# Optimization experiments

Hardware: AMD Instinct MI355X
Metric: run time of the kernel (lower is better)

## Reference

```python
import jax, jax.numpy as jnp
import numpy as np

NEG_SLOPE = 0.2
MASK_FILL = -9e10


def setup_inputs() -> dict:
    key = jax.random.key(0)
    ks = jax.random.split(key, 9)
    B, n_ope, n_mac = 32, 2048, 1024
    total = 64
    ope_dim, mac_dim, out_dim = 64, 64, 128
    ope_ma_adj = jax.random.randint(ks[0], (total, n_ope, n_mac), 0, 2, dtype=jnp.int32)
    batch_idxes = jax.random.randint(ks[1], (B,), 0, total, dtype=jnp.int64)
    feat_ope = jax.random.normal(ks[2], (B, n_ope, ope_dim), dtype=jnp.float32)
    feat_mac = jax.random.normal(ks[3], (B, n_mac, mac_dim), dtype=jnp.float32)
    # parameters (xavier-normal-like scaling)
    def xavier(k, shape):
        fan_in, fan_out = shape[1], shape[0]
        std = jnp.sqrt(2.0 / (fan_in + fan_out))
        return std * jax.random.normal(k, shape, dtype=jnp.float32)
    ope_w = xavier(ks[4], (out_dim, ope_dim))   # Linear weight [out, in]
    mac_w = xavier(ks[5], (out_dim, mac_dim))
    ope_alpha = xavier(ks[6], (out_dim, 1))
    mac_alpha = xavier(ks[7], (out_dim, 1))
    res_w = xavier(ks[8], (out_dim, mac_dim))
    return {
        "ope_ma_adj": ope_ma_adj, "batch_idxes": batch_idxes,
        "feat_ope": feat_ope, "feat_mac": feat_mac,
        "ope_w": ope_w, "mac_w": mac_w,
        "ope_alpha": ope_alpha, "mac_alpha": mac_alpha, "res_w": res_w,
    }


def reference(ope_ma_adj, batch_idxes, feat_ope, feat_mac,
              ope_w, mac_w, ope_alpha, mac_alpha, res_w):
    # dropout p=0 -> identity
    h_ope = jnp.einsum('bod,kd->bok', feat_ope, ope_w)   # [B, n_ope, out]
    h_mac = jnp.einsum('bmd,kd->bmk', feat_mac, mac_w)   # [B, n_mac, out]
    attn_ope = jnp.einsum('bok,k->bo', h_ope, ope_alpha[:, 0])  # [B, n_ope]
    attn_mac = jnp.einsum('bmk,k->bm', h_mac, mac_alpha[:, 0])  # [B, n_mac]
    e = attn_ope[:, :, None] + attn_mac[:, None, :]             # [B, n_ope, n_mac]
    e = jnp.where(e >= 0, e, NEG_SLOPE * e)                      # leaky relu
    mask = ope_ma_adj[batch_idxes] == 1                          # [B, n_ope, n_mac]
    e = jnp.where(mask, e, MASK_FILL)
    alpha = jax.nn.softmax(e, axis=-2)                           # over operations
    out = jnp.einsum('bom,bok->bmk', alpha, h_ope)               # [B, n_mac, out]
    h_res = jnp.einsum('bmd,kd->bmk', feat_mac, res_w)
    return out + h_res
```

## Files before the change

kernel.cpp:

```cpp
#include <hip/hip_runtime.h>

#define N_OPE 2048
#define N_MAC 1024
#define DIM   64
#define KOUT  128
#define NB    32

typedef __attribute__((ext_vector_type(8))) short short8;
typedef __attribute__((ext_vector_type(4))) float floatx4;

static __device__ __forceinline__ unsigned short f2bf(float f) {
    unsigned int u = __builtin_bit_cast(unsigned int, f);
    u += 0x7fffu + ((u >> 16) & 1u);
    return (unsigned short)(u >> 16);
}
static __device__ __forceinline__ float bf2f(unsigned short h) {
    unsigned int u = ((unsigned int)h) << 16;
    return __builtin_bit_cast(float, u);
}

__global__ __launch_bounds__(256, 2) void k_ope(const float* __restrict__ feat,
        const float* __restrict__ w, const float* __restrict__ alpha,
        unsigned short* __restrict__ h_t, float2* __restrict__ pq)
{
    int wid = threadIdx.x >> 6, lane = threadIdx.x & 63;
    int L = lane & 15, q = lane >> 4;
    int base = blockIdx.x * 128 + wid * 32;
    int b = base >> 11;
    int o0w = base & (N_OPE - 1);

    float fA[2][2][8];
    #pragma unroll
    for (int mf = 0; mf < 2; ++mf) {
        const float* fr = feat + (size_t)(base + mf * 16 + L) * DIM + q * 8;
        #pragma unroll
        for (int ks = 0; ks < 2; ++ks) {
            float4 v0 = *(const float4*)(fr + ks * 32);
            float4 v1 = *(const float4*)(fr + ks * 32 + 4);
            fA[mf][ks][0] = v0.x; fA[mf][ks][1] = v0.y; fA[mf][ks][2] = v0.z; fA[mf][ks][3] = v0.w;
            fA[mf][ks][4] = v1.x; fA[mf][ks][5] = v1.y; fA[mf][ks][6] = v1.z; fA[mf][ks][7] = v1.w;
        }
    }

    short8 Ah[2][2], Al[2][2];
    #pragma unroll
    for (int mf = 0; mf < 2; ++mf)
        #pragma unroll
        for (int ks = 0; ks < 2; ++ks)
            #pragma unroll
            for (int j = 0; j < 8; ++j) {
                float x = fA[mf][ks][j];
                unsigned short h = f2bf(x);
                Ah[mf][ks][j] = (short)h;
                Al[mf][ks][j] = (short)f2bf(x - bf2f(h));
            }

    floatx4 C[2][8];
    #pragma unroll
    for (int mf = 0; mf < 2; ++mf)
        #pragma unroll
        for (int nf = 0; nf < 8; ++nf) C[mf][nf] = (floatx4)0.f;

    #pragma unroll
    for (int ks = 0; ks < 2; ++ks) {
        #pragma unroll
        for (int nf = 0; nf < 8; ++nf) {
            const float* wp = w + (size_t)(nf * 16 + L) * DIM + ks * 32 + q * 8;
            float4 u0 = *(const float4*)(wp);
            float4 u1 = *(const float4*)(wp + 4);
            float bw[8] = {u0.x, u0.y, u0.z, u0.w, u1.x, u1.y, u1.z, u1.w};
            short8 Bh, Bl;
            #pragma unroll
            for (int j = 0; j < 8; ++j) {
                unsigned short h = f2bf(bw[j]);
                Bh[j] = (short)h;
                Bl[j] = (short)f2bf(bw[j] - bf2f(h));
            }
            #pragma unroll
            for (int mf = 0; mf < 2; ++mf) {
                C[mf][nf] = __builtin_amdgcn_mfma_f32_16x16x32_bf16(Ah[mf][ks], Bh, C[mf][nf], 0, 0, 0);
                C[mf][nf] = __builtin_amdgcn_mfma_f32_16x16x32_bf16(Al[mf][ks], Bh, C[mf][nf], 0, 0, 0);
                C[mf][nf] = __builtin_amdgcn_mfma_f32_16x16x32_bf16(Ah[mf][ks], Bl, C[mf][nf], 0, 0, 0);
            }
        }
    }

    float alf[8];
    #pragma unroll
    for (int nf = 0; nf < 8; ++nf) alf[nf] = alpha[nf * 16 + L];
    #pragma unroll
    for (int mf = 0; mf < 2; ++mf) {
        #pragma unroll
        for (int r = 0; r < 4; ++r) {
            float s = 0.f;
            #pragma unroll
            for (int nf = 0; nf < 8; ++nf) s = fmaf(C[mf][nf][r], alf[nf], s);
            s += __shfl_xor(s, 1); s += __shfl_xor(s, 2);
            s += __shfl_xor(s, 4); s += __shfl_xor(s, 8);
            if (L == 0)
                pq[base + mf * 16 + q * 4 + r] = make_float2(__expf(s), __expf(0.2f * s));
        }
    }

    __shared__ unsigned short T[4][128 * 34];
    #pragma unroll
    for (int mf = 0; mf < 2; ++mf)
        #pragma unroll
        for (int nf = 0; nf < 8; ++nf)
            #pragma unroll
            for (int r = 0; r < 4; ++r)
                T[wid][(nf * 16 + L) * 34 + mf * 16 + q * 4 + r] = f2bf(C[mf][nf][r]);
    __syncthreads();
    unsigned short* htb = h_t + (size_t)b * KOUT * N_OPE;
    #pragma unroll 4
    for (int t = 0; t < 32; ++t) {
        int n = t * 4 + q;
        ushort2 v = *(const ushort2*)&T[wid][n * 34 + 2 * L];
        *(ushort2*)(htb + (size_t)n * N_OPE + o0w + 2 * L) = v;
    }
}

__global__ __launch_bounds__(256, 3) void k_attn(const int* __restrict__ adj,
        const int* __restrict__ bidx,
        const unsigned short* __restrict__ h_t,
        const float2* __restrict__ pq,
        const float* __restrict__ feat_mac,
        const float* __restrict__ mac_w, const float* __restrict__ mac_alpha,
        const float* __restrict__ res_w,
        float* __restrict__ out)
{
    int b  = blockIdx.y;
    int m0 = blockIdx.x * 32;
    int t  = threadIdx.x;
    int wv = t >> 6;
    int lane = t & 63;
    int L = lane & 15, q = lane >> 4;

    __shared__ float buf0[32 * 132];
    __shared__ float buf1[32 * 132];
    __shared__ float waS[64];
    __shared__ float amS[32];
    __shared__ float DS[4][32];

    {
        int d = t & 63, seg = t >> 6;
        float p = 0.f;
        #pragma unroll 8
        for (int n = seg * 32; n < seg * 32 + 32; ++n)
            p = fmaf(mac_w[n * DIM + d], mac_alpha[n], p);
        buf0[seg * 64 + d] = p;
    }
    __syncthreads();
    if (t < 64) waS[t] = buf0[t] + buf0[64 + t] + buf0[128 + t] + buf0[192 + t];
    __syncthreads();
    {
        int row = t & 31, seg = t >> 5;
        const float* fr = feat_mac + ((size_t)b * N_MAC + m0 + row) * DIM + seg * 8;
        float p = 0.f;
        #pragma unroll
        for (int k = 0; k < 8; ++k) p = fmaf(fr[k], waS[seg * 8 + k], p);
        buf1[seg * 32 + row] = p;
    }
    __syncthreads();
    if (t < 32) {
        float s = 0.f;
        #pragma unroll
        for (int sg = 0; sg < 8; ++sg) s += buf1[sg * 32 + t];
        amS[t] = s;
    }
    __syncthreads();

    float am0 = amS[L], am1 = amS[16 + L];
    float pM0 = __expf(am0), qM0 = __expf(0.2f * am0);
    float pM1 = __expf(am1), qM1 = __expf(0.2f * am1);

    const int* adjt = adj + (size_t)bidx[b] * N_OPE * N_MAC;
    const unsigned short* htb = h_t + (size_t)b * KOUT * N_OPE;
    const float2* pqb = pq + (size_t)b * N_OPE;

    floatx4 C0[8], C1[8];
    #pragma unroll
    for (int i = 0; i < 8; ++i) { C0[i] = (floatx4)0.f; C1[i] = (floatx4)0.f; }
    float den0 = 0.f, den1 = 0.f;

    int oBeg = wv * (N_OPE / 4);
    for (int o0 = oBeg; o0 < oBeg + N_OPE / 4; o0 += 32) {
        int ob = o0 + q * 8;
        float4 pv0 = *(const float4*)(pqb + ob);
        float4 pv1 = *(const float4*)(pqb + ob + 2);
        float4 pv2 = *(const float4*)(pqb + ob + 4);
        float4 pv3 = *(const float4*)(pqb + ob + 6);
        float pA[8] = {pv0.x, pv0.z, pv1.x, pv1.z, pv2.x, pv2.z, pv3.x, pv3.z};
        float qA[8] = {pv0.y, pv0.w, pv1.y, pv1.w, pv2.y, pv2.w, pv3.y, pv3.w};

        short8 Bf[8];
        #pragma unroll
        for (int nf = 0; nf < 8; ++nf)
            Bf[nf] = *(const short8*)(htb + (size_t)(nf * 16 + L) * N_OPE + ob);

        int mk0[8], mk1[8];
        #pragma unroll
        for (int j = 0; j < 8; ++j) {
            mk0[j] = adjt[(size_t)(ob + j) * N_MAC + m0 + L];
            mk1[j] = adjt[(size_t)(ob + j) * N_MAC + m0 + 16 + L];
        }

        float w0v[8], w1v[8];
        #pragma unroll
        for (int j = 0; j < 8; ++j) {
            float tp0 = pA[j] * pM0;
            float w0 = (tp0 >= 1.0f) ? tp0 : qA[j] * qM0;
            w0 = (mk0[j] == 1) ? w0 : 0.f;
            den0 += w0; w0v[j] = w0;
            float tp1 = pA[j] * pM1;
            float w1 = (tp1 >= 1.0f) ? tp1 : qA[j] * qM1;
            w1 = (mk1[j] == 1) ? w1 : 0.f;
            den1 += w1; w1v[j] = w1;
        }
        int4 A0i, A1i;
        #pragma unroll
        for (int j2 = 0; j2 < 4; ++j2) {
            unsigned lo0 = __builtin_bit_cast(unsigned, w0v[2 * j2])     + 0x8000u;
            unsigned hi0 = __builtin_bit_cast(unsigned, w0v[2 * j2 + 1]) + 0x8000u;
            ((unsigned*)&A0i)[j2] = __builtin_amdgcn_perm(hi0, lo0, 0x07060302u);
            unsigned lo1 = __builtin_bit_cast(unsigned, w1v[2 * j2])     + 0x8000u;
            unsigned hi1 = __builtin_bit_cast(unsigned, w1v[2 * j2 + 1]) + 0x8000u;
            ((unsigned*)&A1i)[j2] = __builtin_amdgcn_perm(hi1, lo1, 0x07060302u);
        }
        short8 A0 = __builtin_bit_cast(short8, A0i);
        short8 A1 = __builtin_bit_cast(short8, A1i);

        #pragma unroll
        for (int nf = 0; nf < 8; ++nf) {
            C0[nf] = __builtin_amdgcn_mfma_f32_16x16x32_bf16(A0, Bf[nf], C0[nf], 0, 0, 0);
            C1[nf] = __builtin_amdgcn_mfma_f32_16x16x32_bf16(A1, Bf[nf], C1[nf], 0, 0, 0);
        }
    }

    den0 += __shfl_xor(den0, 16); den0 += __shfl_xor(den0, 32);
    den1 += __shfl_xor(den1, 16); den1 += __shfl_xor(den1, 32);
    if (q == 0) { DS[wv][L] = den0; DS[wv][16 + L] = den1; }

    if (wv == 0 || wv == 2) {
        float* bp = (wv == 0) ? buf0 : buf1;
        #pragma unroll
        for (int mf = 0; mf < 2; ++mf) {
            const floatx4* Cf = mf ? C1 : C0;
            #pragma unroll
            for (int nf = 0; nf < 8; ++nf)
                #pragma unroll
                for (int r = 0; r < 4; ++r)
                    bp[(mf * 16 + q * 4 + r) * 132 + nf * 16 + L] = Cf[nf][r];
        }
    }
    __syncthreads();
    if (wv == 1 || wv == 3) {
        float* bp = (wv == 1) ? buf0 : buf1;
        #pragma unroll
        for (int mf = 0; mf < 2; ++mf) {
            const floatx4* Cf = mf ? C1 : C0;
            #pragma unroll
            for (int nf = 0; nf < 8; ++nf)
                #pragma unroll
                for (int r = 0; r < 4; ++r)
                    bp[(mf * 16 + q * 4 + r) * 132 + nf * 16 + L] += Cf[nf][r];
        }
    }
    __syncthreads();

    float fA[2][2][8];
    #pragma unroll
    for (int mf = 0; mf < 2; ++mf) {
        const float* fr = feat_mac + ((size_t)b * N_MAC + m0 + mf * 16 + L) * DIM + q * 8;
        #pragma unroll
        for (int ks = 0; ks < 2; ++ks) {
            float4 v0 = *(const float4*)(fr + ks * 32);
            float4 v1 = *(const float4*)(fr + ks * 32 + 4);
            fA[mf][ks][0] = v0.x; fA[mf][ks][1] = v0.y; fA[mf][ks][2] = v0.z; fA[mf][ks][3] = v0.w;
            fA[mf][ks][4] = v1.x; fA[mf][ks][5] = v1.y; fA[mf][ks][6] = v1.z; fA[mf][ks][7] = v1.w;
        }
    }
    short8 Ah[2][2], Al[2][2];
    #pragma unroll
    for (int mf = 0; mf < 2; ++mf)
        #pragma unroll
        for (int ks = 0; ks < 2; ++ks)
            #pragma unroll
            for (int j = 0; j < 8; ++j) {
                float x = fA[mf][ks][j];
                unsigned short h = f2bf(x);
                Ah[mf][ks][j] = (short)h;
                Al[mf][ks][j] = (short)f2bf(x - bf2f(h));
            }
    floatx4 R[2][2];
    R[0][0] = (floatx4)0.f; R[0][1] = (floatx4)0.f;
    R[1][0] = (floatx4)0.f; R[1][1] = (floatx4)0.f;
    #pragma unroll
    for (int ks = 0; ks < 2; ++ks) {
        #pragma unroll
        for (int nfl = 0; nfl < 2; ++nfl) {
            const float* wp = res_w + (size_t)((wv * 2 + nfl) * 16 + L) * DIM + ks * 32 + q * 8;
            float4 u0 = *(const float4*)(wp);
            float4 u1 = *(const float4*)(wp + 4);
            float bw[8] = {u0.x, u0.y, u0.z, u0.w, u1.x, u1.y, u1.z, u1.w};
            short8 Bh, Bl;
            #pragma unroll
            for (int j = 0; j < 8; ++j) {
                unsigned short h = f2bf(bw[j]);
                Bh[j] = (short)h;
                Bl[j] = (short)f2bf(bw[j] - bf2f(h));
            }
            #pragma unroll
            for (int mf = 0; mf < 2; ++mf) {
                R[mf][nfl] = __builtin_amdgcn_mfma_f32_16x16x32_bf16(Ah[mf][ks], Bh, R[mf][nfl], 0, 0, 0);
                R[mf][nfl] = __builtin_amdgcn_mfma_f32_16x16x32_bf16(Al[mf][ks], Bh, R[mf][nfl], 0, 0, 0);
                R[mf][nfl] = __builtin_amdgcn_mfma_f32_16x16x32_bf16(Ah[mf][ks], Bl, R[mf][nfl], 0, 0, 0);
            }
        }
    }

    #pragma unroll
    for (int mf = 0; mf < 2; ++mf) {
        #pragma unroll
        for (int r = 0; r < 4; ++r) {
            int row = mf * 16 + q * 4 + r;
            float inv = 1.0f / (DS[0][row] + DS[1][row] + DS[2][row] + DS[3][row]);
            size_t obase = ((size_t)b * N_MAC + m0 + row) * KOUT;
            #pragma unroll
            for (int nfl = 0; nfl < 2; ++nfl) {
                int col = (wv * 2 + nfl) * 16 + L;
                out[obase + col] = (buf0[row * 132 + col] + buf1[row * 132 + col]) * inv
                                   + R[mf][nfl][r];
            }
        }
    }
}

extern "C" void kernel_launch(void* const* d_in, const int* in_sizes, int n_in,
                              void* d_out, int out_size, void* d_ws, size_t ws_size,
                              hipStream_t stream) {
    const int*   adj       = (const int*)d_in[0];
    const int*   bidx      = (const int*)d_in[1];
    const float* feat_ope  = (const float*)d_in[2];
    const float* feat_mac  = (const float*)d_in[3];
    const float* ope_w     = (const float*)d_in[4];
    const float* mac_w     = (const float*)d_in[5];
    const float* ope_alpha = (const float*)d_in[6];
    const float* mac_alpha = (const float*)d_in[7];
    const float* res_w     = (const float*)d_in[8];
    float* out = (float*)d_out;

    char* ws = (char*)d_ws;
    unsigned short* h_t = (unsigned short*)ws;
    float2* pq          = (float2*)(ws + (size_t)(16 << 20));

    k_ope<<<512, 256, 0, stream>>>(feat_ope, ope_w, ope_alpha, h_t, pq);
    k_attn<<<dim3(N_MAC / 32, NB), 256, 0, stream>>>(adj, bidx, h_t, pq, feat_mac,
                                                     mac_w, mac_alpha, res_w, out);
}
```

Baseline: 718.5 us.

## Split mac projection and residual into separate kernels, vectorize adjacency loads

The per-machine attention scalar and the residual projection move out of the attention kernel. A tiny kernel precomputes mac_w^T·mac_alpha, and a new k_mac kernel writes attn_mac plus the residual directly into out. The attention kernel drops its shared-memory prologue and residual MFMA tail; it now adds into out and loads adjacency as int2, with each lane owning two adjacent machine columns. The grid becomes a 1D launch with a remapped batch order and relaxed launch bounds. The cost is two extra launches and an extra read-modify-write of out.

```diff
diff --git a/kernel.cpp b/kernel.cpp
--- a/kernel.cpp
+++ b/kernel.cpp
@@ -17,6 +17,16 @@
 static __device__ __forceinline__ float bf2f(unsigned short h) {
     unsigned int u = ((unsigned int)h) << 16;
     return __builtin_bit_cast(float, u);
+}
+
+__global__ void k_wa(const float* __restrict__ mw, const float* __restrict__ ma,
+                     float* __restrict__ wa)
+{
+    int d = threadIdx.x;
+    float s = 0.f;
+    #pragma unroll 8
+    for (int n = 0; n < KOUT; ++n) s = fmaf(mw[n * DIM + d], ma[n], s);
+    wa[d] = s;
 }
 
 __global__ __launch_bounds__(256, 2) void k_ope(const float* __restrict__ feat,
@@ -120,63 +130,122 @@
     }
 }
 
-__global__ __launch_bounds__(256, 3) void k_attn(const int* __restrict__ adj,
+__global__ __launch_bounds__(256, 2) void k_mac(const float* __restrict__ feat,
+        const float* __restrict__ w, const float* __restrict__ wa,
+        float* __restrict__ out, float* __restrict__ attn)
+{
+    int wid = threadIdx.x >> 6, lane = threadIdx.x & 63;
+    int L = lane & 15, q = lane >> 4;
+    int base = blockIdx.x * 128 + wid * 32;
+
+    float fA[2][2][8];
+    #pragma unroll
+    for (int mf = 0; mf < 2; ++mf) {
+        const float* fr = feat + (size_t)(base + mf * 16 + L) * DIM + q * 8;
+        #pragma unroll
+        for (int ks = 0; ks < 2; ++ks) {
+            float4 v0 = *(const float4*)(fr + ks * 32);
+            float4 v1 = *(const float4*)(fr + ks * 32 + 4);
+            fA[mf][ks][0] = v0.x; fA[mf][ks][1] = v0.y; fA[mf][ks][2] = v0.z; fA[mf][ks][3] = v0.w;
+            fA[mf][ks][4] = v1.x; fA[mf][ks][5] = v1.y; fA[mf][ks][6] = v1.z; fA[mf][ks][7] = v1.w;
+        }
+    }
+
+    float wav[2][8];
+    #pragma unroll
+    for (int ks = 0; ks < 2; ++ks) {
+        float4 w0 = *(const float4*)(wa + ks * 32 + q * 8);
+        float4 w1 = *(const float4*)(wa + ks * 32 + q * 8 + 4);
+        wav[ks][0] = w0.x; wav[ks][1] = w0.y; wav[ks][2] = w0.z; wav[ks][3] = w0.w;
+        wav[ks][4] = w1.x; wav[ks][5] = w1.y; wav[ks][6] = w1.z; wav[ks][7] = w1.w;
+    }
+    float part[2] = {0.f, 0.f};
+    #pragma unroll
+    for (int mf = 0; mf < 2; ++mf)
+        #pragma unroll
+        for (int ks = 0; ks < 2; ++ks)
+            #pragma unroll
+            for (int j = 0; j < 8; ++j)
+                part[mf] = fmaf(fA[mf][ks][j], wav[ks][j], part[mf]);
+    part[0] += __shfl_xor(part[0], 16); part[0] += __shfl_xor(part[0], 32);
+    part[1] += __shfl_xor(part[1], 16); part[1] += __shfl_xor(part[1], 32);
+    if (q == 0) {
+        attn[base + L]      = part[0];
+        attn[base + 16 + L] = part[1];
+    }
+
+    short8 Ah[2][2], Al[2][2];
+    #pragma unroll
+    for (int mf = 0; mf < 2; ++mf)
+        #pragma unroll
+        for (int ks = 0; ks < 2; ++ks)
+            #pragma unroll
+            for (int j = 0; j < 8; ++j) {
+                float x = fA[mf][ks][j];
+                unsigned short h = f2bf(x);
+                Ah[mf][ks][j] = (short)h;
+                Al[mf][ks][j] = (short)f2bf(x - bf2f(h));
+            }
+
+    floatx4 C[2][8];
+    #pragma unroll
+    for (int mf = 0; mf < 2; ++mf)
+        #pragma unroll
+        for (int nf = 0; nf < 8; ++nf) C[mf][nf] = (floatx4)0.f;
+
+    #pragma unroll
+    for (int ks = 0; ks < 2; ++ks) {
+        #pragma unroll
+        for (int nf = 0; nf < 8; ++nf) {
+            const float* wp = w + (size_t)(nf * 16 + L) * DIM + ks * 32 + q * 8;
+            float4 u0 = *(const float4*)(wp);
+            float4 u1 = *(const float4*)(wp + 4);
+            float bw[8] = {u0.x, u0.y, u0.z, u0.w, u1.x, u1.y, u1.z, u1.w};
+            short8 Bh, Bl;
+            #pragma unroll
+            for (int j = 0; j < 8; ++j) {
+                unsigned short h = f2bf(bw[j]);
+                Bh[j] = (short)h;
+                Bl[j] = (short)f2bf(bw[j] - bf2f(h));
+            }
+            #pragma unroll
+            for (int mf = 0; mf < 2; ++mf) {
+                C[mf][nf] = __builtin_amdgcn_mfma_f32_16x16x32_bf16(Ah[mf][ks], Bh, C[mf][nf], 0, 0, 0);
+                C[mf][nf] = __builtin_amdgcn_mfma_f32_16x16x32_bf16(Al[mf][ks], Bh, C[mf][nf], 0, 0, 0);
+                C[mf][nf] = __builtin_amdgcn_mfma_f32_16x16x32_bf16(Ah[mf][ks], Bl, C[mf][nf], 0, 0, 0);
+            }
+        }
+    }
+
+    #pragma unroll
+    for (int mf = 0; mf < 2; ++mf)
+        #pragma unroll
+        for (int nf = 0; nf < 8; ++nf)
+            #pragma unroll
+            for (int r = 0; r < 4; ++r)
+                out[(size_t)(base + mf * 16 + q * 4 + r) * KOUT + nf * 16 + L] = C[mf][nf][r];
+}
+
+__global__ __launch_bounds__(256) void k_attn(const int* __restrict__ adj,
         const int* __restrict__ bidx,
         const unsigned short* __restrict__ h_t,
         const float2* __restrict__ pq,
-        const float* __restrict__ feat_mac,
-        const float* __restrict__ mac_w, const float* __restrict__ mac_alpha,
-        const float* __restrict__ res_w,
+        const float* __restrict__ attn_mac,
         float* __restrict__ out)
 {
-    int b  = blockIdx.y;
-    int m0 = blockIdx.x * 32;
-    int t  = threadIdx.x;
-    int wv = t >> 6;
-    int lane = t & 63;
+    int lin = blockIdx.x;
+    int b   = 4 * (lin & 7) + ((lin >> 3) & 3);
+    int m0  = (lin >> 5) * 32;
+    int t = threadIdx.x, wv = t >> 6, lane = t & 63;
     int L = lane & 15, q = lane >> 4;
 
-    __shared__ float buf0[32 * 132];
-    __shared__ float buf1[32 * 132];
-    __shared__ float waS[64];
-    __shared__ float amS[32];
-    __shared__ float DS[4][32];
-
-    {
-        int d = t & 63, seg = t >> 6;
-        float p = 0.f;
-        #pragma unroll 8
-        for (int n = seg * 32; n < seg * 32 + 32; ++n)
-            p = fmaf(mac_w[n * DIM + d], mac_alpha[n], p);
-        buf0[seg * 64 + d] = p;
-    }
-    __syncthreads();
-    if (t < 64) waS[t] = buf0[t] + buf0[64 + t] + buf0[128 + t] + buf0[192 + t];
-    __syncthreads();
-    {
-        int row = t & 31, seg = t >> 5;
-        const float* fr = feat_mac + ((size_t)b * N_MAC + m0 + row) * DIM + seg * 8;
-        float p = 0.f;
-        #pragma unroll
-        for (int k = 0; k < 8; ++k) p = fmaf(fr[k], waS[seg * 8 + k], p);
-        buf1[seg * 32 + row] = p;
-    }
-    __syncthreads();
-    if (t < 32) {
-        float s = 0.f;
-        #pragma unroll
-        for (int sg = 0; sg < 8; ++sg) s += buf1[sg * 32 + t];
-        amS[t] = s;
-    }
-    __syncthreads();
-
-    float am0 = amS[L], am1 = amS[16 + L];
-    float pM0 = __expf(am0), qM0 = __expf(0.2f * am0);
-    float pM1 = __expf(am1), qM1 = __expf(0.2f * am1);
-
-    const int* adjt = adj + (size_t)bidx[b] * N_OPE * N_MAC;
+    const int* adjt = adj + (size_t)bidx[b] * (N_OPE * N_MAC);
     const unsigned short* htb = h_t + (size_t)b * KOUT * N_OPE;
     const float2* pqb = pq + (size_t)b * N_OPE;
+
+    float2 amv = *(const float2*)(attn_mac + (size_t)b * N_MAC + m0 + 2 * L);
+    float pM0 = __expf(amv.x), qM0 = __expf(0.2f * amv.x);
+    float pM1 = __expf(amv.y), qM1 = __expf(0.2f * amv.y);
 
     floatx4 C0[8], C1[8];
     #pragma unroll
@@ -193,28 +262,26 @@
         float pA[8] = {pv0.x, pv0.z, pv1.x, pv1.z, pv2.x, pv2.z, pv3.x, pv3.z};
         float qA[8] = {pv0.y, pv0.w, pv1.y, pv1.w, pv2.y, pv2.w, pv3.y, pv3.w};
 
+        int2 mk[8];
+        #pragma unroll
+        for (int j = 0; j < 8; ++j)
+            mk[j] = *(const int2*)(adjt + (size_t)(ob + j) * N_MAC + m0 + 2 * L);
+
         short8 Bf[8];
         #pragma unroll
         for (int nf = 0; nf < 8; ++nf)
             Bf[nf] = *(const short8*)(htb + (size_t)(nf * 16 + L) * N_OPE + ob);
-
-        int mk0[8], mk1[8];
-        #pragma unroll
-        for (int j = 0; j < 8; ++j) {
-            mk0[j] = adjt[(size_t)(ob + j) * N_MAC + m0 + L];
-            mk1[j] = adjt[(size_t)(ob + j) * N_MAC + m0 + 16 + L];
-        }
 
         float w0v[8], w1v[8];
         #pragma unroll
         for (int j = 0; j < 8; ++j) {
             float tp0 = pA[j] * pM0;
             float w0 = (tp0 >= 1.0f) ? tp0 : qA[j] * qM0;
-            w0 = (mk0[j] == 1) ? w0 : 0.f;
+            w0 = (mk[j].x == 1) ? w0 : 0.f;
             den0 += w0; w0v[j] = w0;
             float tp1 = pA[j] * pM1;
             float w1 = (tp1 >= 1.0f) ? tp1 : qA[j] * qM1;
-            w1 = (mk1[j] == 1) ? w1 : 0.f;
+            w1 = (mk[j].y == 1) ? w1 : 0.f;
             den1 += w1; w1v[j] = w1;
         }
         int4 A0i, A1i;
@@ -239,6 +306,10 @@
 
     den0 += __shfl_xor(den0, 16); den0 += __shfl_xor(den0, 32);
     den1 += __shfl_xor(den1, 16); den1 += __shfl_xor(den1, 32);
+
+    __shared__ float buf0[32 * 132];
+    __shared__ float buf1[32 * 132];
+    __shared__ float DS[4][32];
     if (q == 0) { DS[wv][L] = den0; DS[wv][16 + L] = den1; }
 
     if (wv == 0 || wv == 2) {
@@ -268,69 +339,21 @@
     }
     __syncthreads();
 
-    float fA[2][2][8];
     #pragma unroll
     for (int mf = 0; mf < 2; ++mf) {
-        const float* fr = feat_mac + ((size_t)b * N_MAC + m0 + mf * 16 + L) * DIM + q * 8;
-        #pragma unroll
-        for (int ks = 0; ks < 2; ++ks) {
-            float4 v0 = *(const float4*)(fr + ks * 32);
-            float4 v1 = *(const float4*)(fr + ks * 32 + 4);
-            fA[mf][ks][0] = v0.x; fA[mf][ks][1] = v0.y; fA[mf][ks][2] = v0.z; fA[mf][ks][3] = v0.w;
-            fA[mf][ks][4] = v1.x; fA[mf][ks][5] = v1.y; fA[mf][ks][6] = v1.z; fA[mf][ks][7] = v1.w;
-        }
-    }
-    short8 Ah[2][2], Al[2][2];
-    #pragma unroll
-    for (int mf = 0; mf < 2; ++mf)
-        #pragma unroll
-        for (int ks = 0; ks < 2; ++ks)
-            #pragma unroll
-            for (int j = 0; j < 8; ++j) {
-                float x = fA[mf][ks][j];
-                unsigned short h = f2bf(x);
-                Ah[mf][ks][j] = (short)h;
-                Al[mf][ks][j] = (short)f2bf(x - bf2f(h));
-            }
-    floatx4 R[2][2];
-    R[0][0] = (floatx4)0.f; R[0][1] = (floatx4)0.f;
-    R[1][0] = (floatx4)0.f; R[1][1] = (floatx4)0.f;
-    #pragma unroll
-    for (int ks = 0; ks < 2; ++ks) {
-        #pragma unroll
-        for (int nfl = 0; nfl < 2; ++nfl) {
-            const float* wp = res_w + (size_t)((wv * 2 + nfl) * 16 + L) * DIM + ks * 32 + q * 8;
-            float4 u0 = *(const float4*)(wp);
-            float4 u1 = *(const float4*)(wp + 4);
-            float bw[8] = {u0.x, u0.y, u0.z, u0.w, u1.x, u1.y, u1.z, u1.w};
-            short8 Bh, Bl;
-            #pragma unroll
-            for (int j = 0; j < 8; ++j) {
-                unsigned short h = f2bf(bw[j]);
-                Bh[j] = (short)h;
-                Bl[j] = (short)f2bf(bw[j] - bf2f(h));
-            }
-            #pragma unroll
-            for (int mf = 0; mf < 2; ++mf) {
-                R[mf][nfl] = __builtin_amdgcn_mfma_f32_16x16x32_bf16(Ah[mf][ks], Bh, R[mf][nfl], 0, 0, 0);
-                R[mf][nfl] = __builtin_amdgcn_mfma_f32_16x16x32_bf16(Al[mf][ks], Bh, R[mf][nfl], 0, 0, 0);
-                R[mf][nfl] = __builtin_amdgcn_mfma_f32_16x16x32_bf16(Ah[mf][ks], Bl, R[mf][nfl], 0, 0, 0);
-            }
-        }
-    }
-
-    #pragma unroll
-    for (int mf = 0; mf < 2; ++mf) {
         #pragma unroll
         for (int r = 0; r < 4; ++r) {
-            int row = mf * 16 + q * 4 + r;
-            float inv = 1.0f / (DS[0][row] + DS[1][row] + DS[2][row] + DS[3][row]);
-            size_t obase = ((size_t)b * N_MAC + m0 + row) * KOUT;
+            int fragrow = q * 4 + r;
+            int m = m0 + 2 * fragrow + mf;
+            float inv = 1.0f / (DS[0][mf * 16 + fragrow] + DS[1][mf * 16 + fragrow]
+                              + DS[2][mf * 16 + fragrow] + DS[3][mf * 16 + fragrow]);
+            size_t obase = ((size_t)b * N_MAC + m) * KOUT;
             #pragma unroll
             for (int nfl = 0; nfl < 2; ++nfl) {
                 int col = (wv * 2 + nfl) * 16 + L;
-                out[obase + col] = (buf0[row * 132 + col] + buf1[row * 132 + col]) * inv
-                                   + R[mf][nfl][r];
+                float num = buf0[(mf * 16 + fragrow) * 132 + col]
+                          + buf1[(mf * 16 + fragrow) * 132 + col];
+                out[obase + col] = num * inv + out[obase + col];
             }
         }
     }
@@ -353,8 +376,11 @@
     char* ws = (char*)d_ws;
     unsigned short* h_t = (unsigned short*)ws;
     float2* pq          = (float2*)(ws + (size_t)(16 << 20));
-
+    float*  attn_mac    = (float*)(ws + (size_t)(16 << 20) + (512 << 10));
+    float*  wa          = (float*)(ws + (size_t)(16 << 20) + (640 << 10));
+
+    k_wa<<<1, 64, 0, stream>>>(mac_w, mac_alpha, wa);
     k_ope<<<512, 256, 0, stream>>>(feat_ope, ope_w, ope_alpha, h_t, pq);
-    k_attn<<<dim3(N_MAC / 32, NB), 256, 0, stream>>>(adj, bidx, h_t, pq, feat_mac,
-                                                     mac_w, mac_alpha, res_w, out);
-}
+    k_mac<<<256, 256, 0, stream>>>(feat_mac, res_w, wa, out, attn_mac);
+    k_attn<<<1024, 256, 0, stream>>>(adj, bidx, h_t, pq, attn_mac, out);
+}
```

Measured after the change: 740.5 us. 3.1% more time.

## Store h_ope in MFMA fragment layout and load adjacency as int2 pairs

Applied to the files above, without the earlier changes.

k_ope now writes the bf16 projected operation features pre-swizzled into the MFMA B-fragment order, so each lane in k_attn does one contiguous 16-byte load per fragment instead of strided row gathers. The machine rows handled by a lane are remapped to interleaved pairs (2L, 2L+1) so the adjacency mask is read as one 8-byte int2 per operation row instead of two scalar loads. The residual and output indexing are adjusted to the new row mapping, and the occupancy hint on k_attn is relaxed. The cost is extra complexity in the remapped indexing and a different LDS padding in k_ope.

```diff
diff --git a/kernel.cpp b/kernel.cpp
--- a/kernel.cpp
+++ b/kernel.cpp
@@ -21,7 +21,7 @@
 
 __global__ __launch_bounds__(256, 2) void k_ope(const float* __restrict__ feat,
         const float* __restrict__ w, const float* __restrict__ alpha,
-        unsigned short* __restrict__ h_t, float2* __restrict__ pq)
+        unsigned short* __restrict__ h_f, float2* __restrict__ pq)
 {
     int wid = threadIdx.x >> 6, lane = threadIdx.x & 63;
     int L = lane & 15, q = lane >> 4;
@@ -102,27 +102,28 @@
         }
     }
 
-    __shared__ unsigned short T[4][128 * 34];
+    __shared__ unsigned short T[4][128 * 40];
     #pragma unroll
     for (int mf = 0; mf < 2; ++mf)
         #pragma unroll
         for (int nf = 0; nf < 8; ++nf)
             #pragma unroll
             for (int r = 0; r < 4; ++r)
-                T[wid][(nf * 16 + L) * 34 + mf * 16 + q * 4 + r] = f2bf(C[mf][nf][r]);
-    __syncthreads();
-    unsigned short* htb = h_t + (size_t)b * KOUT * N_OPE;
-    #pragma unroll 4
-    for (int t = 0; t < 32; ++t) {
-        int n = t * 4 + q;
-        ushort2 v = *(const ushort2*)&T[wid][n * 34 + 2 * L];
-        *(ushort2*)(htb + (size_t)n * N_OPE + o0w + 2 * L) = v;
-    }
-}
-
-__global__ __launch_bounds__(256, 3) void k_attn(const int* __restrict__ adj,
+                T[wid][(nf * 16 + L) * 40 + mf * 16 + q * 4 + r] = f2bf(C[mf][nf][r]);
+    __syncthreads();
+
+    int oc = o0w >> 5;
+    unsigned short* dst = h_f + ((((size_t)b * 64 + oc) * 8) * 64 + lane) * 8;
+    #pragma unroll
+    for (int nf = 0; nf < 8; ++nf) {
+        short8 v = *(const short8*)&T[wid][(nf * 16 + L) * 40 + q * 8];
+        *(short8*)(dst + (size_t)nf * 512) = v;
+    }
+}
+
+__global__ __launch_bounds__(256) void k_attn(const int* __restrict__ adj,
         const int* __restrict__ bidx,
-        const unsigned short* __restrict__ h_t,
+        const unsigned short* __restrict__ h_f,
         const float2* __restrict__ pq,
         const float* __restrict__ feat_mac,
         const float* __restrict__ mac_w, const float* __restrict__ mac_alpha,
@@ -131,9 +132,7 @@
 {
     int b  = blockIdx.y;
     int m0 = blockIdx.x * 32;
-    int t  = threadIdx.x;
-    int wv = t >> 6;
-    int lane = t & 63;
+    int t = threadIdx.x, wv = t >> 6, lane = t & 63;
     int L = lane & 15, q = lane >> 4;
 
     __shared__ float buf0[32 * 132];
@@ -170,12 +169,12 @@
     }
     __syncthreads();
 
-    float am0 = amS[L], am1 = amS[16 + L];
-    float pM0 = __expf(am0), qM0 = __expf(0.2f * am0);
-    float pM1 = __expf(am1), qM1 = __expf(0.2f * am1);
-
-    const int* adjt = adj + (size_t)bidx[b] * N_OPE * N_MAC;
-    const unsigned short* htb = h_t + (size_t)b * KOUT * N_OPE;
+    float2 amv = *(const float2*)&amS[2 * L];
+    float pM0 = __expf(amv.x), qM0 = __expf(0.2f * amv.x);
+    float pM1 = __expf(amv.y), qM1 = __expf(0.2f * amv.y);
+
+    const int* adjt = adj + (size_t)bidx[b] * (N_OPE * N_MAC);
+    const unsigned short* hfb = h_f + (size_t)b * (64 * 8 * 64 * 8);
     const float2* pqb = pq + (size_t)b * N_OPE;
 
     floatx4 C0[8], C1[8];
@@ -193,28 +192,27 @@
         float pA[8] = {pv0.x, pv0.z, pv1.x, pv1.z, pv2.x, pv2.z, pv3.x, pv3.z};
         float qA[8] = {pv0.y, pv0.w, pv1.y, pv1.w, pv2.y, pv2.w, pv3.y, pv3.w};
 
+        int2 mk[8];
+        #pragma unroll
+        for (int j = 0; j < 8; ++j)
+            mk[j] = *(const int2*)(adjt + (size_t)(ob + j) * N_MAC + m0 + 2 * L);
+
+        const unsigned short* fp = hfb + (((size_t)(o0 >> 5) * 8) * 64 + lane) * 8;
         short8 Bf[8];
         #pragma unroll
         for (int nf = 0; nf < 8; ++nf)
-            Bf[nf] = *(const short8*)(htb + (size_t)(nf * 16 + L) * N_OPE + ob);
-
-        int mk0[8], mk1[8];
-        #pragma unroll
-        for (int j = 0; j < 8; ++j) {
-            mk0[j] = adjt[(size_t)(ob + j) * N_MAC + m0 + L];
-            mk1[j] = adjt[(size_t)(ob + j) * N_MAC + m0 + 16 + L];
-        }
+            Bf[nf] = *(const short8*)(fp + (size_t)nf * 512);
 
         float w0v[8], w1v[8];
         #pragma unroll
         for (int j = 0; j < 8; ++j) {
             float tp0 = pA[j] * pM0;
             float w0 = (tp0 >= 1.0f) ? tp0 : qA[j] * qM0;
-            w0 = (mk0[j] == 1) ? w0 : 0.f;
+            w0 = (mk[j].x == 1) ? w0 : 0.f;
             den0 += w0; w0v[j] = w0;
             float tp1 = pA[j] * pM1;
             float w1 = (tp1 >= 1.0f) ? tp1 : qA[j] * qM1;
-            w1 = (mk1[j] == 1) ? w1 : 0.f;
+            w1 = (mk[j].y == 1) ? w1 : 0.f;
             den1 += w1; w1v[j] = w1;
         }
         int4 A0i, A1i;
@@ -271,7 +269,7 @@
     float fA[2][2][8];
     #pragma unroll
     for (int mf = 0; mf < 2; ++mf) {
-        const float* fr = feat_mac + ((size_t)b * N_MAC + m0 + mf * 16 + L) * DIM + q * 8;
+        const float* fr = feat_mac + ((size_t)b * N_MAC + m0 + 2 * L + mf) * DIM + q * 8;
         #pragma unroll
         for (int ks = 0; ks < 2; ++ks) {
             float4 v0 = *(const float4*)(fr + ks * 32);
@@ -323,14 +321,17 @@
     for (int mf = 0; mf < 2; ++mf) {
         #pragma unroll
         for (int r = 0; r < 4; ++r) {
-            int row = mf * 16 + q * 4 + r;
-            float inv = 1.0f / (DS[0][row] + DS[1][row] + DS[2][row] + DS[3][row]);
-            size_t obase = ((size_t)b * N_MAC + m0 + row) * KOUT;
+            int fragrow = q * 4 + r;
+            int m = m0 + 2 * fragrow + mf;
+            float inv = 1.0f / (DS[0][mf * 16 + fragrow] + DS[1][mf * 16 + fragrow]
+                              + DS[2][mf * 16 + fragrow] + DS[3][mf * 16 + fragrow]);
+            size_t obase = ((size_t)b * N_MAC + m) * KOUT;
             #pragma unroll
             for (int nfl = 0; nfl < 2; ++nfl) {
                 int col = (wv * 2 + nfl) * 16 + L;
-                out[obase + col] = (buf0[row * 132 + col] + buf1[row * 132 + col]) * inv
-                                   + R[mf][nfl][r];
+                float num = buf0[(mf * 16 + fragrow) * 132 + col]
+                          + buf1[(mf * 16 + fragrow) * 132 + col];
+                out[obase + col] = num * inv + R[mf][nfl][r];
             }
         }
     }
@@ -351,10 +352,10 @@
     float* out = (float*)d_out;
 
     char* ws = (char*)d_ws;
-    unsigned short* h_t = (unsigned short*)ws;
+    unsigned short* h_f = (unsigned short*)ws;
     float2* pq          = (float2*)(ws + (size_t)(16 << 20));
 
-    k_ope<<<512, 256, 0, stream>>>(feat_ope, ope_w, ope_alpha, h_t, pq);
-    k_attn<<<dim3(N_MAC / 32, NB), 256, 0, stream>>>(adj, bidx, h_t, pq, feat_mac,
+    k_ope<<<512, 256, 0, stream>>>(feat_ope, ope_w, ope_alpha, h_f, pq);
+    k_attn<<<dim3(N_MAC / 32, NB), 256, 0, stream>>>(adj, bidx, h_f, pq, feat_mac,
                                                      mac_w, mac_alpha, res_w, out);
 }
```

Result: faster. 695.0 us (-3.3%).
